# Kernel tuning notes

Measured on AMD Instinct MI355X. Metric: run time of the kernel, lower is better.

## Reference

```python
import jax, jax.numpy as jnp
import numpy as np

B, S, D, H, K = 64, 512, 1024, 1024, 4
DT = 0.05
TAU_MIN, TAU_MAX = 0.01, 10.0


def setup_inputs() -> dict:
    key = jax.random.key(0)
    ks = jax.random.split(key, 5)
    x = jax.random.normal(ks[0], (B, S, D), dtype=jnp.float32)
    # complexity signal [B,1]; positive like a variance
    complexity = jax.random.uniform(ks[1], (B, 1), dtype=jnp.float32) + 0.5
    # orthogonal-ish recurrent weight (scaled normal) and xavier-ish input weight
    W_rec = jax.random.normal(ks[2], (H, H), dtype=jnp.float32) / np.float32(np.sqrt(H))
    W_in = jax.random.normal(ks[3], (D, H), dtype=jnp.float32) * np.float32(np.sqrt(2.0 / (D + H)))
    bias = jnp.zeros((H,), dtype=jnp.float32)
    tau_bands = jnp.logspace(np.log10(TAU_MIN), np.log10(TAU_MAX), K, dtype=jnp.float32)
    mixer_w = jax.random.normal(ks[4], (K, 1), dtype=jnp.float32)  # nn.Linear(1, K).weight
    mixer_b = jnp.zeros((K,), dtype=jnp.float32)                   # nn.Linear(1, K).bias
    return dict(x=x, complexity=complexity, W_rec=W_rec, W_in=W_in,
                bias=bias, tau_bands=tau_bands, mixer_w=mixer_w, mixer_b=mixer_b)


def reference(x, complexity, W_rec, W_in, bias, tau_bands, mixer_w, mixer_b):
    # tau mixing: Linear(1,K) on complexity -> softmax -> convex mix of tau bands
    tau_logits = complexity @ mixer_w.T + mixer_b          # [B, K]
    w = jax.nn.softmax(tau_logits, axis=-1)                # [B, K]
    mixed_tau = jnp.sum(tau_bands[None, :] * w, axis=1)    # [B]
    alpha = jnp.exp(-DT / mixed_tau)[:, None]              # [B, 1] -> broadcasts over H

    h0 = jnp.zeros((x.shape[0], W_rec.shape[0]), dtype=x.dtype)

    def step(h, xt):
        # h_{t+1} = a*h + (1-a)*tanh(h @ W_rec^T + x_t @ W_in^T + b)
        pre = h @ W_rec.T + xt @ W_in.T + bias
        h_new = alpha * h + (1.0 - alpha) * jnp.tanh(pre)
        return h_new, h_new

    h_final, outs = jax.lax.scan(step, h0, jnp.swapaxes(x, 0, 1))  # scan over time
    output = jnp.swapaxes(outs, 0, 1)                               # [B, S, H]
    return output, h_final
```

## Files before the change

kernel.cpp:

```cpp
#include <hip/hip_runtime.h>
#include <math.h>

#define BATCH 64
#define SEQ 512
#define DIM 1024
#define HID 1024
#define KBANDS 4
#define DT_C 0.05f
#define CNT_STRIDE 32

__global__ void alpha_kernel(const float* __restrict__ complexity,
                             const float* __restrict__ tau_bands,
                             const float* __restrict__ mixer_w,
                             const float* __restrict__ mixer_b,
                             float* __restrict__ alpha) {
    int b = threadIdx.x;
    if (b < BATCH) {
        float c = complexity[b];
        float lg[KBANDS];
        float mx = -1e30f;
        #pragma unroll
        for (int k = 0; k < KBANDS; k++) {
            lg[k] = c * mixer_w[k] + mixer_b[k];
            mx = fmaxf(mx, lg[k]);
        }
        float se = 0.f, tau = 0.f;
        #pragma unroll
        for (int k = 0; k < KBANDS; k++) {
            float e = expf(lg[k] - mx);
            se += e;
            tau += tau_bands[k] * e;
        }
        tau /= se;
        alpha[b] = expf(-DT_C / tau);
    }
}

#define BM 64
#define BN 64
#define BK 16
__global__ __launch_bounds__(256) void in_gemm(const float* __restrict__ x,
                                               const float* __restrict__ Win,
                                               const float* __restrict__ bias,
                                               float* __restrict__ out) {
    __shared__ float As[BK][BM + 4];
    __shared__ float Bs[BK][BN + 4];
    int tid = threadIdx.x;
    int tx = tid & 15, ty = tid >> 4;
    int m0 = blockIdx.x * BM;
    int n0 = blockIdx.y * BN;
    float c[4][4] = {};
    int lmm = tid >> 2;
    int lkq = (tid & 3) * 4;
    for (int k0 = 0; k0 < 1024; k0 += BK) {
        float4 a4 = *(const float4*)(x + (size_t)(m0 + lmm) * 1024 + k0 + lkq);
        float4 b4 = *(const float4*)(Win + (size_t)(n0 + lmm) * 1024 + k0 + lkq);
        As[lkq + 0][lmm] = a4.x; As[lkq + 1][lmm] = a4.y;
        As[lkq + 2][lmm] = a4.z; As[lkq + 3][lmm] = a4.w;
        Bs[lkq + 0][lmm] = b4.x; Bs[lkq + 1][lmm] = b4.y;
        Bs[lkq + 2][lmm] = b4.z; Bs[lkq + 3][lmm] = b4.w;
        __syncthreads();
        #pragma unroll
        for (int kk = 0; kk < BK; kk++) {
            float a[4], bb[4];
            #pragma unroll
            for (int i = 0; i < 4; i++) a[i] = As[kk][ty * 4 + i];
            #pragma unroll
            for (int j = 0; j < 4; j++) bb[j] = Bs[kk][tx * 4 + j];
            #pragma unroll
            for (int i = 0; i < 4; i++)
                #pragma unroll
                for (int j = 0; j < 4; j++)
                    c[i][j] += a[i] * bb[j];
        }
        __syncthreads();
    }
    int n = n0 + tx * 4;
    float4 bias4 = *(const float4*)(bias + n);
    #pragma unroll
    for (int i = 0; i < 4; i++) {
        int m = m0 + ty * 4 + i;
        float4 st;
        st.x = c[i][0] + bias4.x;
        st.y = c[i][1] + bias4.y;
        st.z = c[i][2] + bias4.z;
        st.w = c[i][3] + bias4.w;
        *(float4*)(out + (size_t)m * 1024 + n) = st;
    }
}


#define HPITCH 2064
#define LDS_HI  0
#define LDS_LO  33024
#define LDS_RED 66048
#define LDS_TOTAL 70144
#define HB_PLANE 131072
#define HB_PARITY 262144

typedef short bf16x8 __attribute__((ext_vector_type(8)));
typedef float f32x4 __attribute__((ext_vector_type(4)));

__device__ __forceinline__ unsigned bf16rn(float x) {
    unsigned u = __float_as_uint(x);
    return (u + 0x7fffu + ((u >> 16) & 1u)) >> 16;
}

__device__ __forceinline__ void splitf(float f, unsigned short* hi, unsigned short* lo) {
    unsigned h = bf16rn(f);
    float r = f - __uint_as_float(h << 16);
    *hi = (unsigned short)h;
    *lo = (unsigned short)bf16rn(r);
}

__global__ __launch_bounds__(256, 1) void recur_coop(const float* __restrict__ Wrec,
                                                     const float* __restrict__ alpha,
                                                     float* __restrict__ out,
                                                     int* __restrict__ cnt,
                                                     unsigned short* __restrict__ hbuf) {
    extern __shared__ char lbase[];

    int tid  = threadIdx.x;
    int bs   = blockIdx.x & 3;
    int js   = blockIdx.x >> 2;
    int lane = tid & 63;
    int w    = tid >> 6;
    int row  = lane & 15;
    int kq   = lane >> 4;

    bf16x8 wh[8], wl[8];
    {
        const float* wsrc = Wrec + (size_t)(js * 16 + row) * HID + w * 256 + kq * 8;
        #pragma unroll
        for (int ks = 0; ks < 8; ks++) {
            float4 f0 = *(const float4*)(wsrc + ks * 32);
            float4 f1 = *(const float4*)(wsrc + ks * 32 + 4);
            union { unsigned short u[8]; bf16x8 v; } H, L;
            splitf(f0.x, &H.u[0], &L.u[0]);
            splitf(f0.y, &H.u[1], &L.u[1]);
            splitf(f0.z, &H.u[2], &L.u[2]);
            splitf(f0.w, &H.u[3], &L.u[3]);
            splitf(f1.x, &H.u[4], &L.u[4]);
            splitf(f1.y, &H.u[5], &L.u[5]);
            splitf(f1.z, &H.u[6], &L.u[6]);
            splitf(f1.w, &H.u[7], &L.u[7]);
            wh[ks] = H.v;
            wl[ks] = L.v;
        }
    }

    int eb = tid >> 4;
    int ej = tid & 15;
    int bglob = bs * 16 + eb;
    int jglob = js * 16 + ej;
    float a_reg = alpha[bglob];
    float om = 1.f - a_reg;
    float* xwp = out + (size_t)bglob * SEQ * HID + jglob;

    int srow = tid >> 4, sl16 = tid & 15;
    const char* hb_lane = (const char*)hbuf + (size_t)(bs * 16 + srow) * 2048 + sl16 * 16;
    char* ph_base = (char*)hbuf + (size_t)bglob * 2048 + jglob * 2;

    float hp = 0.f;
    float* redp = (float*)(lbase + LDS_RED);
    const char* ah_base = lbase + LDS_HI + row * HPITCH + (w * 256 + kq * 8) * 2;
    const char* al_base = lbase + LDS_LO + row * HPITCH + (w * 256 + kq * 8) * 2;
    char* dh = lbase + LDS_HI + srow * HPITCH + sl16 * 16;
    char* dl = lbase + LDS_LO + srow * HPITCH + sl16 * 16;

    for (int t = 0; t < SEQ; t++) {
        float xw = *xwp;
        float sum = 0.f;
        if (t > 0) {
            if (tid == 0) {
                int* cp = cnt + (size_t)((t - 1) * 4 + bs) * CNT_STRIDE;
                int spins = 0;
                while (__hip_atomic_load(cp, __ATOMIC_RELAXED,
                                         __HIP_MEMORY_SCOPE_AGENT) < 64) {
                    __builtin_amdgcn_s_sleep(1);
                    if (++spins >= 8192) {
                        spins = 0;
                        if (__hip_atomic_fetch_add(cp, 0, __ATOMIC_RELAXED,
                                __HIP_MEMORY_SCOPE_AGENT) >= 64) break;
                    }
                }
            }
            __syncthreads();
            {
                const char* bh = hb_lane + (size_t)((t - 1) & 1) * HB_PARITY;
                const char* bl = bh + HB_PLANE;
                float4 v[16];
                #pragma unroll
                for (int it = 0; it < 8; it++)
                    asm volatile("global_load_dwordx4 %0, %1, off offset:%2 sc0 sc1"
                                 : "=v"(v[it]) : "v"(bh), "i"(it * 256) : "memory");
                #pragma unroll
                for (int it = 0; it < 8; it++)
                    asm volatile("global_load_dwordx4 %0, %1, off offset:%2 sc0 sc1"
                                 : "=v"(v[8 + it]) : "v"(bl), "i"(it * 256) : "memory");
                asm volatile("s_waitcnt vmcnt(0)" ::: "memory");
                #pragma unroll
                for (int it = 0; it < 8; it++)
                    *(float4*)(dh + it * 256) = v[it];
                #pragma unroll
                for (int it = 0; it < 8; it++)
                    *(float4*)(dl + it * 256) = v[8 + it];
            }
            __syncthreads();
            f32x4 acc0 = {0.f, 0.f, 0.f, 0.f};
            f32x4 acc1 = {0.f, 0.f, 0.f, 0.f};
            #pragma unroll
            for (int ks = 0; ks < 8; ks++) {
                bf16x8 ah = *(const bf16x8*)(ah_base + ks * 64);
                bf16x8 al = *(const bf16x8*)(al_base + ks * 64);
                if (ks & 1) {
                    acc1 = __builtin_amdgcn_mfma_f32_16x16x32_bf16(ah, wh[ks], acc1, 0, 0, 0);
                    acc1 = __builtin_amdgcn_mfma_f32_16x16x32_bf16(al, wh[ks], acc1, 0, 0, 0);
                    acc1 = __builtin_amdgcn_mfma_f32_16x16x32_bf16(ah, wl[ks], acc1, 0, 0, 0);
                } else {
                    acc0 = __builtin_amdgcn_mfma_f32_16x16x32_bf16(ah, wh[ks], acc0, 0, 0, 0);
                    acc0 = __builtin_amdgcn_mfma_f32_16x16x32_bf16(al, wh[ks], acc0, 0, 0, 0);
                    acc0 = __builtin_amdgcn_mfma_f32_16x16x32_bf16(ah, wl[ks], acc0, 0, 0, 0);
                }
            }
            #pragma unroll
            for (int r = 0; r < 4; r++)
                redp[w * 256 + (kq * 4 + r) * 16 + row] = acc0[r] + acc1[r];
            __syncthreads();
            sum = redp[tid] + redp[256 + tid] + redp[512 + tid] + redp[768 + tid];
        }
        float pre = sum + xw;
        float hn = a_reg * hp + om * tanhf(pre);
        *xwp = hn;
        if (t == SEQ - 1)
            out[(size_t)BATCH * SEQ * HID + (size_t)bglob * HID + jglob] = hn;
        {
            unsigned short hi16, lo16;
            splitf(hn, &hi16, &lo16);
            unsigned hv = hi16, lv = lo16;
            char* ph = ph_base + (size_t)(t & 1) * HB_PARITY;
            char* pl = ph + HB_PLANE;
            asm volatile("global_store_short %0, %1, off sc0 sc1"
                         :: "v"(ph), "v"(hv) : "memory");
            asm volatile("global_store_short %0, %1, off sc0 sc1"
                         :: "v"(pl), "v"(lv) : "memory");
        }
        asm volatile("s_waitcnt vmcnt(0)" ::: "memory");
        __syncthreads();
        if (tid == 0)
            __hip_atomic_fetch_add(cnt + (size_t)(t * 4 + bs) * CNT_STRIDE, 1,
                    __ATOMIC_RELAXED, __HIP_MEMORY_SCOPE_AGENT);
        hp = hn;
        xwp += HID;
    }
}

extern "C" void kernel_launch(void* const* d_in, const int* in_sizes, int n_in,
                              void* d_out, int out_size, void* d_ws, size_t ws_size,
                              hipStream_t stream) {
    const float* x          = (const float*)d_in[0];
    const float* complexity = (const float*)d_in[1];
    const float* Wrec       = (const float*)d_in[2];
    const float* Win        = (const float*)d_in[3];
    const float* bias       = (const float*)d_in[4];
    const float* tau_bands  = (const float*)d_in[5];
    const float* mixer_w    = (const float*)d_in[6];
    const float* mixer_b    = (const float*)d_in[7];
    float* out = (float*)d_out;

    float* alpha = (float*)d_ws;
    int*   cnt   = (int*)((char*)d_ws + 256);
    unsigned short* hbuf = (unsigned short*)((char*)d_ws + 266240);

    hipMemsetAsync(cnt, 0, SEQ * 4 * CNT_STRIDE * sizeof(int), stream);
    alpha_kernel<<<1, 64, 0, stream>>>(complexity, tau_bands, mixer_w, mixer_b, alpha);
    in_gemm<<<dim3(32768 / BM, 1024 / BN), 256, 0, stream>>>(x, Win, bias, out);

    hipFuncSetAttribute((const void*)recur_coop,
                        hipFuncAttributeMaxDynamicSharedMemorySize, LDS_TOTAL);
    void* args[] = { (void*)&Wrec, (void*)&alpha, (void*)&out, (void*)&cnt, (void*)&hbuf };
    hipLaunchCooperativeKernel((void*)recur_coop, dim3(256), dim3(256),
                               args, LDS_TOTAL, stream);
}
```

Before: 2.871 ms.

## Replace per-step atomic counter with per-block flags and per-wave waits

Each producer block now publishes its progress by storing the timestep into its own flag instead of incrementing a shared per-step counter. Each wave polls only the 16 flags for the producer blocks whose h slices it needs and waits on them with a wave-wide vote, then loads its own slice into LDS without block-wide barriers. This removes the atomic contention and the two __syncthreads per step on the consumer side. The cost is more polling traffic and careful memory ordering, since the flag stores are relaxed and there is no block barrier before the MFMA reads.

```diff
diff --git a/kernel.cpp b/kernel.cpp
--- a/kernel.cpp
+++ b/kernel.cpp
@@ -7,7 +7,6 @@
 #define HID 1024
 #define KBANDS 4
 #define DT_C 0.05f
-#define CNT_STRIDE 32
 
 __global__ void alpha_kernel(const float* __restrict__ complexity,
                              const float* __restrict__ tau_bands,
@@ -157,35 +156,42 @@
     float om = 1.f - a_reg;
     float* xwp = out + (size_t)bglob * SEQ * HID + jglob;
 
-    int srow = tid >> 4, sl16 = tid & 15;
-    const char* hb_lane = (const char*)hbuf + (size_t)(bs * 16 + srow) * 2048 + sl16 * 16;
+    int srow = lane >> 2;
+    int sk4  = lane & 3;
+    const char* hb_lane = (const char*)hbuf
+        + (size_t)(bs * 16 + srow) * 2048 + w * 512 + sk4 * 128;
     char* ph_base = (char*)hbuf + (size_t)bglob * 2048 + jglob * 2;
 
-    float hp = 0.f;
-    float* redp = (float*)(lbase + LDS_RED);
+    char* dh = lbase + LDS_HI + srow * HPITCH + w * 512 + sk4 * 128;
+    char* dl = lbase + LDS_LO + srow * HPITCH + w * 512 + sk4 * 128;
     const char* ah_base = lbase + LDS_HI + row * HPITCH + (w * 256 + kq * 8) * 2;
     const char* al_base = lbase + LDS_LO + row * HPITCH + (w * 256 + kq * 8) * 2;
-    char* dh = lbase + LDS_HI + srow * HPITCH + sl16 * 16;
-    char* dl = lbase + LDS_LO + srow * HPITCH + sl16 * 16;
+    float* redp = (float*)(lbase + LDS_RED);
+
+    int* myflag = cnt + bs * 64 + w * 16 + (lane & 15);
+
+    float hp = 0.f;
 
     for (int t = 0; t < SEQ; t++) {
         float xw = *xwp;
         float sum = 0.f;
         if (t > 0) {
-            if (tid == 0) {
-                int* cp = cnt + (size_t)((t - 1) * 4 + bs) * CNT_STRIDE;
+            {
                 int spins = 0;
-                while (__hip_atomic_load(cp, __ATOMIC_RELAXED,
-                                         __HIP_MEMORY_SCOPE_AGENT) < 64) {
+                for (;;) {
+                    int v = __hip_atomic_load(myflag, __ATOMIC_RELAXED,
+                                              __HIP_MEMORY_SCOPE_AGENT);
+                    if (__all(v >= t)) break;
                     __builtin_amdgcn_s_sleep(1);
-                    if (++spins >= 8192) {
+                    if (++spins >= 16384) {
                         spins = 0;
-                        if (__hip_atomic_fetch_add(cp, 0, __ATOMIC_RELAXED,
-                                __HIP_MEMORY_SCOPE_AGENT) >= 64) break;
+                        v = __hip_atomic_fetch_add(myflag, 0, __ATOMIC_RELAXED,
+                                                   __HIP_MEMORY_SCOPE_AGENT);
+                        if (__all(v >= t)) break;
                     }
                 }
             }
-            __syncthreads();
+            __builtin_amdgcn_sched_barrier(0);
             {
                 const char* bh = hb_lane + (size_t)((t - 1) & 1) * HB_PARITY;
                 const char* bl = bh + HB_PLANE;
@@ -193,20 +199,21 @@
                 #pragma unroll
                 for (int it = 0; it < 8; it++)
                     asm volatile("global_load_dwordx4 %0, %1, off offset:%2 sc0 sc1"
-                                 : "=v"(v[it]) : "v"(bh), "i"(it * 256) : "memory");
+                                 : "=v"(v[it]) : "v"(bh), "i"(it * 16) : "memory");
                 #pragma unroll
                 for (int it = 0; it < 8; it++)
                     asm volatile("global_load_dwordx4 %0, %1, off offset:%2 sc0 sc1"
-                                 : "=v"(v[8 + it]) : "v"(bl), "i"(it * 256) : "memory");
+                                 : "=v"(v[8 + it]) : "v"(bl), "i"(it * 16) : "memory");
                 asm volatile("s_waitcnt vmcnt(0)" ::: "memory");
                 #pragma unroll
                 for (int it = 0; it < 8; it++)
-                    *(float4*)(dh + it * 256) = v[it];
-                #pragma unroll
-                for (int it = 0; it < 8; it++)
-                    *(float4*)(dl + it * 256) = v[8 + it];
+                    *(float4*)(dh + it * 16) = v[it];
+                #pragma unroll
+                for (int it = 0; it < 8; it++)
+                    *(float4*)(dl + it * 16) = v[8 + it];
             }
-            __syncthreads();
+            asm volatile("s_waitcnt lgkmcnt(0)" ::: "memory");
+            __builtin_amdgcn_sched_barrier(0);
             f32x4 acc0 = {0.f, 0.f, 0.f, 0.f};
             f32x4 acc1 = {0.f, 0.f, 0.f, 0.f};
             #pragma unroll
@@ -248,8 +255,8 @@
         asm volatile("s_waitcnt vmcnt(0)" ::: "memory");
         __syncthreads();
         if (tid == 0)
-            __hip_atomic_fetch_add(cnt + (size_t)(t * 4 + bs) * CNT_STRIDE, 1,
-                    __ATOMIC_RELAXED, __HIP_MEMORY_SCOPE_AGENT);
+            __hip_atomic_store(cnt + bs * 64 + js, t + 1, __ATOMIC_RELAXED,
+                               __HIP_MEMORY_SCOPE_AGENT);
         hp = hn;
         xwp += HID;
     }
@@ -272,7 +279,7 @@
     int*   cnt   = (int*)((char*)d_ws + 256);
     unsigned short* hbuf = (unsigned short*)((char*)d_ws + 266240);
 
-    hipMemsetAsync(cnt, 0, SEQ * 4 * CNT_STRIDE * sizeof(int), stream);
+    hipMemsetAsync(cnt, 0, 256 * sizeof(int), stream);
     alpha_kernel<<<1, 64, 0, stream>>>(complexity, tau_bands, mixer_w, mixer_b, alpha);
     in_gemm<<<dim3(32768 / BM, 1024 / BN), 256, 0, stream>>>(x, Win, bias, out);
 
```

New measurement: 5.333 ms. 85.8% more time.

## Split per-step barrier into per-wave counters over column groups

Applied to the files above, without the earlier changes.

Each of the 64 blocks per batch slice now signals a counter keyed by its group of 16 column-blocks. Each wave waits only on the group that produced the 256-column slice of h it consumes, then loads that slice into LDS itself. This removes two block-wide __syncthreads per step and lets waves start their MFMA slice as soon as their producers finish. The counter array grows fourfold and hbuf moves to make room. Correctness relies on each wave reading only the LDS rows it wrote, which holds because each wave reads its own K-range.

```diff
diff --git a/kernel.cpp b/kernel.cpp
--- a/kernel.cpp
+++ b/kernel.cpp
@@ -96,7 +96,7 @@
 #define LDS_RED 66048
 #define LDS_TOTAL 70144
 #define HB_PLANE 131072
-#define HB_PARITY 262144
+#define HB_SLOT  262144
 
 typedef short bf16x8 __attribute__((ext_vector_type(8)));
 typedef float f32x4 __attribute__((ext_vector_type(4)));
@@ -127,6 +127,7 @@
     int w    = tid >> 6;
     int row  = lane & 15;
     int kq   = lane >> 4;
+    int gself = js >> 4;
 
     bf16x8 wh[8], wl[8];
     {
@@ -157,56 +158,61 @@
     float om = 1.f - a_reg;
     float* xwp = out + (size_t)bglob * SEQ * HID + jglob;
 
-    int srow = tid >> 4, sl16 = tid & 15;
-    const char* hb_lane = (const char*)hbuf + (size_t)(bs * 16 + srow) * 2048 + sl16 * 16;
+    int sr2  = lane >> 5;
+    int sc32 = lane & 31;
+    const char* hb_w = (const char*)hbuf + (size_t)(bs * 16 + sr2) * 2048
+                                   + w * 512 + sc32 * 16;
     char* ph_base = (char*)hbuf + (size_t)bglob * 2048 + jglob * 2;
 
-    float hp = 0.f;
-    float* redp = (float*)(lbase + LDS_RED);
+    char* dh_w = lbase + LDS_HI + sr2 * HPITCH + w * 512 + sc32 * 16;
+    char* dl_w = lbase + LDS_LO + sr2 * HPITCH + w * 512 + sc32 * 16;
     const char* ah_base = lbase + LDS_HI + row * HPITCH + (w * 256 + kq * 8) * 2;
     const char* al_base = lbase + LDS_LO + row * HPITCH + (w * 256 + kq * 8) * 2;
-    char* dh = lbase + LDS_HI + srow * HPITCH + sl16 * 16;
-    char* dl = lbase + LDS_LO + srow * HPITCH + sl16 * 16;
+    float* redp = (float*)(lbase + LDS_RED);
+
+    float hp = 0.f;
 
     for (int t = 0; t < SEQ; t++) {
         float xw = *xwp;
         float sum = 0.f;
         if (t > 0) {
-            if (tid == 0) {
-                int* cp = cnt + (size_t)((t - 1) * 4 + bs) * CNT_STRIDE;
+            if (lane == 0) {
+                int* cp = cnt + (size_t)((t - 1) * 16 + bs * 4 + w) * CNT_STRIDE;
                 int spins = 0;
                 while (__hip_atomic_load(cp, __ATOMIC_RELAXED,
-                                         __HIP_MEMORY_SCOPE_AGENT) < 64) {
+                                         __HIP_MEMORY_SCOPE_AGENT) < 16) {
                     __builtin_amdgcn_s_sleep(1);
                     if (++spins >= 8192) {
                         spins = 0;
                         if (__hip_atomic_fetch_add(cp, 0, __ATOMIC_RELAXED,
-                                __HIP_MEMORY_SCOPE_AGENT) >= 64) break;
+                                __HIP_MEMORY_SCOPE_AGENT) >= 16) break;
                     }
                 }
             }
-            __syncthreads();
             {
-                const char* bh = hb_lane + (size_t)((t - 1) & 1) * HB_PARITY;
+                const char* bh = hb_w + (size_t)((t - 1) & 1) * HB_SLOT;
                 const char* bl = bh + HB_PLANE;
                 float4 v[16];
                 #pragma unroll
+                for (int it = 0; it < 8; it++) {
+                    const char* p = bh + it * 4096;
+                    asm volatile("global_load_dwordx4 %0, %1, off sc0 sc1"
+                                 : "=v"(v[it]) : "v"(p) : "memory");
+                }
+                #pragma unroll
+                for (int it = 0; it < 8; it++) {
+                    const char* p = bl + it * 4096;
+                    asm volatile("global_load_dwordx4 %0, %1, off sc0 sc1"
+                                 : "=v"(v[8 + it]) : "v"(p) : "memory");
+                }
+                asm volatile("s_waitcnt vmcnt(0)" ::: "memory");
+                #pragma unroll
                 for (int it = 0; it < 8; it++)
-                    asm volatile("global_load_dwordx4 %0, %1, off offset:%2 sc0 sc1"
-                                 : "=v"(v[it]) : "v"(bh), "i"(it * 256) : "memory");
+                    *(float4*)(dh_w + it * (2 * HPITCH)) = v[it];
                 #pragma unroll
                 for (int it = 0; it < 8; it++)
-                    asm volatile("global_load_dwordx4 %0, %1, off offset:%2 sc0 sc1"
-                                 : "=v"(v[8 + it]) : "v"(bl), "i"(it * 256) : "memory");
-                asm volatile("s_waitcnt vmcnt(0)" ::: "memory");
-                #pragma unroll
-                for (int it = 0; it < 8; it++)
-                    *(float4*)(dh + it * 256) = v[it];
-                #pragma unroll
-                for (int it = 0; it < 8; it++)
-                    *(float4*)(dl + it * 256) = v[8 + it];
+                    *(float4*)(dl_w + it * (2 * HPITCH)) = v[8 + it];
             }
-            __syncthreads();
             f32x4 acc0 = {0.f, 0.f, 0.f, 0.f};
             f32x4 acc1 = {0.f, 0.f, 0.f, 0.f};
             #pragma unroll
@@ -238,7 +244,7 @@
             unsigned short hi16, lo16;
             splitf(hn, &hi16, &lo16);
             unsigned hv = hi16, lv = lo16;
-            char* ph = ph_base + (size_t)(t & 1) * HB_PARITY;
+            char* ph = ph_base + (size_t)(t & 1) * HB_SLOT;
             char* pl = ph + HB_PLANE;
             asm volatile("global_store_short %0, %1, off sc0 sc1"
                          :: "v"(ph), "v"(hv) : "memory");
@@ -248,8 +254,9 @@
         asm volatile("s_waitcnt vmcnt(0)" ::: "memory");
         __syncthreads();
         if (tid == 0)
-            __hip_atomic_fetch_add(cnt + (size_t)(t * 4 + bs) * CNT_STRIDE, 1,
-                    __ATOMIC_RELAXED, __HIP_MEMORY_SCOPE_AGENT);
+            __hip_atomic_fetch_add(
+                cnt + (size_t)(t * 16 + bs * 4 + gself) * CNT_STRIDE, 1,
+                __ATOMIC_RELAXED, __HIP_MEMORY_SCOPE_AGENT);
         hp = hn;
         xwp += HID;
     }
@@ -270,9 +277,9 @@
 
     float* alpha = (float*)d_ws;
     int*   cnt   = (int*)((char*)d_ws + 256);
-    unsigned short* hbuf = (unsigned short*)((char*)d_ws + 266240);
-
-    hipMemsetAsync(cnt, 0, SEQ * 4 * CNT_STRIDE * sizeof(int), stream);
+    unsigned short* hbuf = (unsigned short*)((char*)d_ws + 256 + 1048576);
+
+    hipMemsetAsync(cnt, 0, SEQ * 16 * CNT_STRIDE * sizeof(int), stream);
     alpha_kernel<<<1, 64, 0, stream>>>(complexity, tau_bands, mixer_w, mixer_b, alpha);
     in_gemm<<<dim3(32768 / BM, 1024 / BN), 256, 0, stream>>>(x, Win, bias, out);
 
```

Result: slower. 3.404 ms (+18.6%).

## Move input projection GEMM to bf16 MFMA with hi/lo split precision

Applied to the files above, without the earlier changes.

Replaces the fp32 SIMT input GEMM with a matrix-core kernel. It splits x and W_in into bf16 hi and lo parts and accumulates three MFMA products to keep near-fp32 accuracy. A small pre-kernel splits W_in once into workspace buffers. This cuts the cost of the large x@W_in^T projection, at the price of extra split work, uncoalesced scalar output stores and a small precision loss.

```diff
diff --git a/kernel.cpp b/kernel.cpp
--- a/kernel.cpp
+++ b/kernel.cpp
@@ -8,6 +8,29 @@
 #define KBANDS 4
 #define DT_C 0.05f
 #define CNT_STRIDE 32
+
+typedef short bf16x8 __attribute__((ext_vector_type(8)));
+typedef float f32x4 __attribute__((ext_vector_type(4)));
+
+__device__ __forceinline__ unsigned bf16rn(float x) {
+    unsigned u = __float_as_uint(x);
+    return (u + 0x7fffu + ((u >> 16) & 1u)) >> 16;
+}
+
+__device__ __forceinline__ void splitf(float f, unsigned short* hi, unsigned short* lo) {
+    unsigned h = bf16rn(f);
+    float r = f - __uint_as_float(h << 16);
+    *hi = (unsigned short)h;
+    *lo = (unsigned short)bf16rn(r);
+}
+
+__device__ __forceinline__ void split_bf16(float4 f, ushort4* hi, ushort4* lo) {
+    unsigned short h0, h1, h2, h3, l0, l1, l2, l3;
+    splitf(f.x, &h0, &l0); splitf(f.y, &h1, &l1);
+    splitf(f.z, &h2, &l2); splitf(f.w, &h3, &l3);
+    *hi = make_ushort4(h0, h1, h2, h3);
+    *lo = make_ushort4(l0, l1, l2, l3);
+}
 
 __global__ void alpha_kernel(const float* __restrict__ complexity,
                              const float* __restrict__ tau_bands,
@@ -36,57 +59,92 @@
     }
 }
 
-#define BM 64
-#define BN 64
-#define BK 16
-__global__ __launch_bounds__(256) void in_gemm(const float* __restrict__ x,
-                                               const float* __restrict__ Win,
-                                               const float* __restrict__ bias,
-                                               float* __restrict__ out) {
-    __shared__ float As[BK][BM + 4];
-    __shared__ float Bs[BK][BN + 4];
-    int tid = threadIdx.x;
-    int tx = tid & 15, ty = tid >> 4;
-    int m0 = blockIdx.x * BM;
-    int n0 = blockIdx.y * BN;
-    float c[4][4] = {};
-    int lmm = tid >> 2;
-    int lkq = (tid & 3) * 4;
-    for (int k0 = 0; k0 < 1024; k0 += BK) {
-        float4 a4 = *(const float4*)(x + (size_t)(m0 + lmm) * 1024 + k0 + lkq);
-        float4 b4 = *(const float4*)(Win + (size_t)(n0 + lmm) * 1024 + k0 + lkq);
-        As[lkq + 0][lmm] = a4.x; As[lkq + 1][lmm] = a4.y;
-        As[lkq + 2][lmm] = a4.z; As[lkq + 3][lmm] = a4.w;
-        Bs[lkq + 0][lmm] = b4.x; Bs[lkq + 1][lmm] = b4.y;
-        Bs[lkq + 2][lmm] = b4.z; Bs[lkq + 3][lmm] = b4.w;
+__global__ __launch_bounds__(256) void win_split(const float* __restrict__ win,
+                                                 unsigned short* __restrict__ whi,
+                                                 unsigned short* __restrict__ wlo) {
+    size_t i = ((size_t)blockIdx.x * 256 + threadIdx.x) * 4;
+    float4 f = *(const float4*)(win + i);
+    ushort4 h4, l4;
+    split_bf16(f, &h4, &l4);
+    *(ushort4*)(whi + i) = h4;
+    *(ushort4*)(wlo + i) = l4;
+}
+
+#define RP 272
+#define IG_LDS (4 * 64 * RP)
+
+__global__ __launch_bounds__(256) void in_gemm_mfma(const float* __restrict__ x,
+                                                    const unsigned short* __restrict__ whi,
+                                                    const unsigned short* __restrict__ wlo,
+                                                    const float* __restrict__ bias,
+                                                    float* __restrict__ out) {
+    extern __shared__ char lg[];
+    char* Ahi = lg;
+    char* Alo = lg + 64 * RP;
+    char* Bhi = lg + 2 * 64 * RP;
+    char* Blo = lg + 3 * 64 * RP;
+
+    int tid  = threadIdx.x;
+    int m0   = blockIdx.x * 64;
+    int n0   = blockIdx.y * 64;
+    int lane = tid & 63;
+    int w    = tid >> 6;
+    int row  = lane & 15;
+    int kq   = lane >> 4;
+
+    int srow = tid >> 2;
+    int skeg = (tid & 3) * 32;
+
+    const float* xsrc = x + (size_t)(m0 + srow) * 1024 + skeg;
+    const unsigned short* bhsrc = whi + (size_t)(n0 + srow) * 1024 + skeg;
+    const unsigned short* blsrc = wlo + (size_t)(n0 + srow) * 1024 + skeg;
+    char* dah = Ahi + srow * RP + skeg * 2;
+    char* dal = Alo + srow * RP + skeg * 2;
+    char* dbh = Bhi + srow * RP + skeg * 2;
+    char* dbl = Blo + srow * RP + skeg * 2;
+
+    f32x4 acc[4];
+    #pragma unroll
+    for (int mt = 0; mt < 4; mt++) acc[mt] = (f32x4){0.f, 0.f, 0.f, 0.f};
+
+    for (int k0 = 0; k0 < 1024; k0 += 128) {
+        #pragma unroll
+        for (int i = 0; i < 8; i++) {
+            float4 f = *(const float4*)(xsrc + k0 + i * 4);
+            ushort4 h4, l4;
+            split_bf16(f, &h4, &l4);
+            *(ushort4*)(dah + i * 8) = h4;
+            *(ushort4*)(dal + i * 8) = l4;
+        }
+        #pragma unroll
+        for (int i = 0; i < 4; i++) {
+            *(float4*)(dbh + i * 16) = *(const float4*)(bhsrc + k0 + i * 8);
+            *(float4*)(dbl + i * 16) = *(const float4*)(blsrc + k0 + i * 8);
+        }
         __syncthreads();
         #pragma unroll
-        for (int kk = 0; kk < BK; kk++) {
-            float a[4], bb[4];
+        for (int ks = 0; ks < 4; ks++) {
+            int koff = (ks * 32 + kq * 8) * 2;
+            bf16x8 bh = *(const bf16x8*)(Bhi + (w * 16 + row) * RP + koff);
+            bf16x8 bl = *(const bf16x8*)(Blo + (w * 16 + row) * RP + koff);
             #pragma unroll
-            for (int i = 0; i < 4; i++) a[i] = As[kk][ty * 4 + i];
-            #pragma unroll
-            for (int j = 0; j < 4; j++) bb[j] = Bs[kk][tx * 4 + j];
-            #pragma unroll
-            for (int i = 0; i < 4; i++)
-                #pragma unroll
-                for (int j = 0; j < 4; j++)
-                    c[i][j] += a[i] * bb[j];
+            for (int mt = 0; mt < 4; mt++) {
+                bf16x8 ah = *(const bf16x8*)(Ahi + (mt * 16 + row) * RP + koff);
+                bf16x8 al = *(const bf16x8*)(Alo + (mt * 16 + row) * RP + koff);
+                acc[mt] = __builtin_amdgcn_mfma_f32_16x16x32_bf16(ah, bh, acc[mt], 0, 0, 0);
+                acc[mt] = __builtin_amdgcn_mfma_f32_16x16x32_bf16(al, bh, acc[mt], 0, 0, 0);
+                acc[mt] = __builtin_amdgcn_mfma_f32_16x16x32_bf16(ah, bl, acc[mt], 0, 0, 0);
+            }
         }
         __syncthreads();
     }
-    int n = n0 + tx * 4;
-    float4 bias4 = *(const float4*)(bias + n);
+    int n = n0 + w * 16 + (lane & 15);
+    float bn = bias[n];
     #pragma unroll
-    for (int i = 0; i < 4; i++) {
-        int m = m0 + ty * 4 + i;
-        float4 st;
-        st.x = c[i][0] + bias4.x;
-        st.y = c[i][1] + bias4.y;
-        st.z = c[i][2] + bias4.z;
-        st.w = c[i][3] + bias4.w;
-        *(float4*)(out + (size_t)m * 1024 + n) = st;
-    }
+    for (int mt = 0; mt < 4; mt++)
+        #pragma unroll
+        for (int r = 0; r < 4; r++)
+            out[(size_t)(m0 + mt * 16 + kq * 4 + r) * 1024 + n] = acc[mt][r] + bn;
 }
 
 
@@ -96,22 +154,7 @@
 #define LDS_RED 66048
 #define LDS_TOTAL 70144
 #define HB_PLANE 131072
-#define HB_PARITY 262144
-
-typedef short bf16x8 __attribute__((ext_vector_type(8)));
-typedef float f32x4 __attribute__((ext_vector_type(4)));
-
-__device__ __forceinline__ unsigned bf16rn(float x) {
-    unsigned u = __float_as_uint(x);
-    return (u + 0x7fffu + ((u >> 16) & 1u)) >> 16;
-}
-
-__device__ __forceinline__ void splitf(float f, unsigned short* hi, unsigned short* lo) {
-    unsigned h = bf16rn(f);
-    float r = f - __uint_as_float(h << 16);
-    *hi = (unsigned short)h;
-    *lo = (unsigned short)bf16rn(r);
-}
+#define HB_SLOT  262144
 
 __global__ __launch_bounds__(256, 1) void recur_coop(const float* __restrict__ Wrec,
                                                      const float* __restrict__ alpha,
@@ -187,7 +230,7 @@
             }
             __syncthreads();
             {
-                const char* bh = hb_lane + (size_t)((t - 1) & 1) * HB_PARITY;
+                const char* bh = hb_lane + (size_t)((t - 1) & 1) * HB_SLOT;
                 const char* bl = bh + HB_PLANE;
                 float4 v[16];
                 #pragma unroll
@@ -238,7 +281,7 @@
             unsigned short hi16, lo16;
             splitf(hn, &hi16, &lo16);
             unsigned hv = hi16, lv = lo16;
-            char* ph = ph_base + (size_t)(t & 1) * HB_PARITY;
+            char* ph = ph_base + (size_t)(t & 1) * HB_SLOT;
             char* pl = ph + HB_PLANE;
             asm volatile("global_store_short %0, %1, off sc0 sc1"
                          :: "v"(ph), "v"(hv) : "memory");
@@ -270,11 +313,17 @@
 
     float* alpha = (float*)d_ws;
     int*   cnt   = (int*)((char*)d_ws + 256);
-    unsigned short* hbuf = (unsigned short*)((char*)d_ws + 266240);
+    unsigned short* whi  = (unsigned short*)((char*)d_ws + 266240);
+    unsigned short* wlo  = (unsigned short*)((char*)d_ws + 266240 + 2097152);
+    unsigned short* hbuf = (unsigned short*)((char*)d_ws + 266240 + 4194304);
 
     hipMemsetAsync(cnt, 0, SEQ * 4 * CNT_STRIDE * sizeof(int), stream);
     alpha_kernel<<<1, 64, 0, stream>>>(complexity, tau_bands, mixer_w, mixer_b, alpha);
-    in_gemm<<<dim3(32768 / BM, 1024 / BN), 256, 0, stream>>>(x, Win, bias, out);
+    win_split<<<1024, 256, 0, stream>>>(Win, whi, wlo);
+
+    hipFuncSetAttribute((const void*)in_gemm_mfma,
+                        hipFuncAttributeMaxDynamicSharedMemorySize, IG_LDS);
+    in_gemm_mfma<<<dim3(512, 16), 256, IG_LDS, stream>>>(x, whi, wlo, bias, out);
 
     hipFuncSetAttribute((const void*)recur_coop,
                         hipFuncAttributeMaxDynamicSharedMemorySize, LDS_TOTAL);
```

Result: faster. 2.544 ms (-11.4%).
